# Kernel tuning notes

Hardware: AMD Instinct MI355X
Metric: run time of the kernel (lower is better)

The kernel has to match this reference:

```python
import jax, jax.numpy as jnp
import numpy as np

N_NODES = 100000
N_EDGES = 1600000
F_IN, F_HID, N_CLS = 128, 128, 16


def setup_inputs() -> dict:
    key = jax.random.key(0)
    ks = jax.random.split(key, 6)
    x = jax.random.normal(ks[0], (N_NODES, F_IN), dtype=jnp.float32)
    edge_index = jax.random.randint(ks[1], (2, N_EDGES), 0, N_NODES, dtype=jnp.int64)
    # Glorot-ish scaled weights (PyG GCNConv uses glorot init, bias zeros)
    W1 = jax.random.normal(ks[2], (F_IN, F_HID), dtype=jnp.float32) * (1.0 / np.sqrt(F_IN))
    b1 = jnp.zeros((F_HID,), dtype=jnp.float32)
    W2 = jax.random.normal(ks[3], (F_HID, N_CLS), dtype=jnp.float32) * (1.0 / np.sqrt(F_HID))
    b2 = jnp.zeros((N_CLS,), dtype=jnp.float32)
    return {"x": x, "edge_index": edge_index, "W1": W1, "b1": b1, "W2": W2, "b2": b2}


def _gcn_conv(x, src, dst, W, b, num_nodes):
    """PyG GCNConv: y = D^{-1/2} (A + I) D^{-1/2} (x W) + b.
    src/dst already include self-loops."""
    h = x @ W  # [N, F_out]
    deg = jax.ops.segment_sum(jnp.ones_like(dst, dtype=h.dtype), dst, num_segments=num_nodes)
    dis = jnp.where(deg > 0, jax.lax.rsqrt(jnp.maximum(deg, 1e-12)), 0.0)
    norm = dis[src] * dis[dst]  # [E+N]
    msg = h[src] * norm[:, None]  # gather + scale  [E+N, F_out]
    out = jax.ops.segment_sum(msg, dst, num_segments=num_nodes)  # scatter-add at targets
    return out + b


def reference(x, edge_index, W1, b1, W2, b2):
    num_nodes = x.shape[0]
    loops = jnp.arange(num_nodes, dtype=edge_index.dtype)
    src = jnp.concatenate([edge_index[0], loops])
    dst = jnp.concatenate([edge_index[1], loops])
    h = _gcn_conv(x, src, dst, W1, b1, num_nodes)
    h = jax.nn.relu(h)
    # F.dropout with training=False (eval mode) is identity
    h = _gcn_conv(h, src, dst, W2, b2, num_nodes)
    return jax.nn.log_softmax(h, axis=1)
```

## Files before the change

### kernel.cpp

```cpp
#include <hip/hip_runtime.h>
#include <math.h>

#define N_NODES 100000
#define N_EDGES 1600000
#define NBINS 391
#define NCHUNK 400
#define CHUNK 4000
#define M_H (NBINS * NCHUNK)
#define NBLK_H 611

typedef __attribute__((ext_vector_type(8))) short bf16x8;
typedef __attribute__((ext_vector_type(4))) float f32x4;
typedef __attribute__((ext_vector_type(2))) float f32x2;

__device__ __forceinline__ unsigned short f2bf(float f) {
    unsigned int u = __float_as_uint(f);
    u += 0x7FFF + ((u >> 16) & 1);
    return (unsigned short)(u >> 16);
}
__device__ __forceinline__ float bf_lo(unsigned int u) { return __uint_as_float(u << 16); }
__device__ __forceinline__ float bf_hi(unsigned int u) { return __uint_as_float(u & 0xFFFF0000u); }
__device__ __forceinline__ f32x2 bfpair(unsigned int u) {
    f32x2 r; r.x = bf_lo(u); r.y = bf_hi(u); return r;
}


__global__ __launch_bounds__(256) void passA_kernel(const int* __restrict__ dst,
                                                    int* __restrict__ H) {
    __shared__ int lh[NBINS];
    int tid = threadIdx.x, c = blockIdx.x;
    for (int i = tid; i < NBINS; i += 256) lh[i] = 0;
    __syncthreads();
    int base = c * CHUNK;
    #pragma unroll
    for (int i = 0; i < 16; ++i) {
        int o = i * 256 + tid;
        if (o < CHUNK) atomicAdd(&lh[dst[base + o] >> 8], 1);
    }
    __syncthreads();
    for (int i = tid; i < NBINS; i += 256) H[i * NCHUNK + c] = lh[i];
}

__global__ __launch_bounds__(256) void scanB1_kernel(int* __restrict__ H,
                                                     int* __restrict__ blk2) {
    __shared__ int s[256];
    int t = threadIdx.x, i = blockIdx.x * 256 + t;
    int v = (i < M_H) ? H[i] : 0;
    s[t] = v;
    __syncthreads();
    for (int off = 1; off < 256; off <<= 1) {
        int u = (t >= off) ? s[t - off] : 0;
        __syncthreads();
        s[t] += u;
        __syncthreads();
    }
    if (i < M_H) H[i] = s[t] - v;
    if (t == 255) blk2[blockIdx.x] = s[255];
}

__global__ __launch_bounds__(1024) void scanB2_kernel(int* __restrict__ blk2) {
    __shared__ int s[1024];
    int t = threadIdx.x;
    int v = (t < NBLK_H) ? blk2[t] : 0;
    s[t] = v;
    __syncthreads();
    for (int off = 1; off < 1024; off <<= 1) {
        int u = (t >= off) ? s[t - off] : 0;
        __syncthreads();
        s[t] += u;
        __syncthreads();
    }
    if (t < NBLK_H) blk2[t] = s[t] - v;
}

__global__ __launch_bounds__(256) void passC_kernel(const int* __restrict__ src,
                                                    const int* __restrict__ dst,
                                                    const int* __restrict__ H,
                                                    const int* __restrict__ blk2,
                                                    int* __restrict__ rec,
                                                    const float* __restrict__ x,
                                                    const float* __restrict__ W1,
                                                    const float* __restrict__ W2,
                                                    ushort* __restrict__ xb,
                                                    ushort* __restrict__ W1T,
                                                    ushort* __restrict__ W2T) {
    int b = blockIdx.x;
    if (b < NCHUNK) {
        __shared__ int base[NBINS];
        __shared__ int rk[NBINS];
        int tid = threadIdx.x;
        for (int i = tid; i < NBINS; i += 256) {
            int idx = i * NCHUNK + b;
            base[i] = H[idx] + blk2[idx >> 8];
            rk[i] = 0;
        }
        __syncthreads();
        int estart = b * CHUNK;
        #pragma unroll
        for (int i = 0; i < 16; ++i) {
            int o = i * 256 + tid;
            if (o < CHUNK) {
                int e = estart + o;
                int d = dst[e];
                int bin = d >> 8;
                int r = atomicAdd(&rk[bin], 1);
                rec[base[bin] + r] = src[e] | ((d & 255) << 17);
            }
        }
    } else if (b < NCHUNK + 12500) {
        int i = (b - NCHUNK) * 256 + threadIdx.x;
        float4 v = *(const float4*)&x[i * 4];
        ushort4 o;
        o.x = f2bf(v.x); o.y = f2bf(v.y); o.z = f2bf(v.z); o.w = f2bf(v.w);
        *(ushort4*)&xb[i * 4] = o;
    } else {
        int j = (b - NCHUNK - 12500) * 256 + threadIdx.x;
        if (j < 16384) {
            int k = j >> 7, n = j & 127;
            W1T[n * 128 + k] = f2bf(W1[j]);
        } else {
            int q = j - 16384;
            int k = q >> 4, n = q & 15;
            W2T[n * 128 + k] = f2bf(W2[q]);
        }
    }
}

__global__ __launch_bounds__(256) void passD_kernel(const int* __restrict__ H,
                                                    const int* __restrict__ blk2,
                                                    const int* __restrict__ rec,
                                                    int* __restrict__ col,
                                                    int* __restrict__ cnt,
                                                    float* __restrict__ dis) {
    __shared__ int fh[256];
    __shared__ int s[256];
    __shared__ int run[256];
    int b = blockIdx.x, t = threadIdx.x;
    int i0 = b * NCHUNK;
    int estart = H[i0] + blk2[i0 >> 8];
    int eend;
    if (b == NBINS - 1) eend = N_EDGES;
    else { int i1 = (b + 1) * NCHUNK; eend = H[i1] + blk2[i1 >> 8]; }
    fh[t] = 0;
    __syncthreads();
    for (int e = estart + t; e < eend; e += 256)
        atomicAdd(&fh[rec[e] >> 17], 1);
    __syncthreads();
    int v = fh[t];
    s[t] = v;
    __syncthreads();
    for (int off = 1; off < 256; off <<= 1) {
        int u = (t >= off) ? s[t - off] : 0;
        __syncthreads();
        s[t] += u;
        __syncthreads();
    }
    int node = b * 256 + t;
    int start = estart + s[t] - v;
    run[t] = start;
    if (node < N_NODES) {
        cnt[node] = start;
        dis[node] = rsqrtf((float)v + 1.0f);
    }
    __syncthreads();
    for (int e = estart + t; e < eend; e += 256) {
        int r = rec[e];
        int p = atomicAdd(&run[r >> 17], 1);
        col[p] = r & 0x1FFFF;
    }
}


__global__ __launch_bounds__(256) void gather1_kernel(const int* __restrict__ col,
                                                      const int* __restrict__ cnt,
                                                      const float* __restrict__ dis,
                                                      const unsigned int* __restrict__ xb,
                                                      unsigned int* __restrict__ xa) {
    int t = threadIdx.x;
    int node = blockIdx.x * 4 + (t >> 6);
    int lane = t & 63;
    float dn = dis[node];
    int beg = cnt[node];
    int end = (node == N_NODES - 1) ? N_EDGES : cnt[node + 1];
    unsigned int su = xb[node * 64 + lane];
    f32x2 a0 = bfpair(su) * dn;
    f32x2 a1 = {0.f, 0.f}, a2 = {0.f, 0.f}, a3 = {0.f, 0.f};
    f32x2 a4 = {0.f, 0.f}, a5 = {0.f, 0.f}, a6 = {0.f, 0.f}, a7 = {0.f, 0.f};
    int k = beg;
    for (; k + 8 <= end; k += 8) {
        int s0 = col[k], s1 = col[k + 1], s2 = col[k + 2], s3 = col[k + 3];
        int s4 = col[k + 4], s5 = col[k + 5], s6 = col[k + 6], s7 = col[k + 7];
        float w0 = dis[s0], w1 = dis[s1], w2 = dis[s2], w3 = dis[s3];
        float w4 = dis[s4], w5 = dis[s5], w6 = dis[s6], w7 = dis[s7];
        unsigned int u0 = xb[s0 * 64 + lane], u1 = xb[s1 * 64 + lane];
        unsigned int u2 = xb[s2 * 64 + lane], u3 = xb[s3 * 64 + lane];
        unsigned int u4 = xb[s4 * 64 + lane], u5 = xb[s5 * 64 + lane];
        unsigned int u6 = xb[s6 * 64 + lane], u7 = xb[s7 * 64 + lane];
        a0 += bfpair(u0) * w0;
        a1 += bfpair(u1) * w1;
        a2 += bfpair(u2) * w2;
        a3 += bfpair(u3) * w3;
        a4 += bfpair(u4) * w4;
        a5 += bfpair(u5) * w5;
        a6 += bfpair(u6) * w6;
        a7 += bfpair(u7) * w7;
    }
    for (; k + 4 <= end; k += 4) {
        int s0 = col[k], s1 = col[k + 1], s2 = col[k + 2], s3 = col[k + 3];
        float w0 = dis[s0], w1 = dis[s1], w2 = dis[s2], w3 = dis[s3];
        unsigned int u0 = xb[s0 * 64 + lane], u1 = xb[s1 * 64 + lane];
        unsigned int u2 = xb[s2 * 64 + lane], u3 = xb[s3 * 64 + lane];
        a0 += bfpair(u0) * w0;
        a1 += bfpair(u1) * w1;
        a2 += bfpair(u2) * w2;
        a3 += bfpair(u3) * w3;
    }
    for (; k < end; ++k) {
        int s = col[k];
        float w = dis[s];
        a0 += bfpair(xb[s * 64 + lane]) * w;
    }
    f32x2 r = (((a0 + a1) + (a2 + a3)) + ((a4 + a5) + (a6 + a7))) * dn;
    xa[node * 64 + lane] = (unsigned int)f2bf(r.x) | ((unsigned int)f2bf(r.y) << 16);
}


__global__ __launch_bounds__(256) void mlp_kernel(const ushort* __restrict__ xa,
                                                  const ushort* __restrict__ W1T,
                                                  const float* __restrict__ b1,
                                                  const ushort* __restrict__ W2T,
                                                  ushort* __restrict__ h2b) {
    __shared__ ushort sh[4][16][136];
    int t = threadIdx.x;
    int wave = t >> 6, lane = t & 63;
    int l = lane & 15, quad = lane >> 4;
    int m0 = blockIdx.x * 64 + wave * 16;
    bool valid = (m0 < N_NODES);
    int row = valid ? (m0 + l) : 0;

    f32x4 acc[8] = {};
    #pragma unroll
    for (int kk = 0; kk < 4; ++kk) {
        bf16x8 a = *(const bf16x8*)&xa[row * 128 + kk * 32 + quad * 8];
        #pragma unroll
        for (int nt = 0; nt < 8; ++nt) {
            bf16x8 b = *(const bf16x8*)&W1T[(nt * 16 + l) * 128 + kk * 32 + quad * 8];
            acc[nt] = __builtin_amdgcn_mfma_f32_16x16x32_bf16(a, b, acc[nt], 0, 0, 0);
        }
    }
    #pragma unroll
    for (int nt = 0; nt < 8; ++nt) {
        float bias = b1[nt * 16 + l];
        #pragma unroll
        for (int r = 0; r < 4; ++r)
            sh[wave][quad * 4 + r][nt * 16 + l] = f2bf(fmaxf(acc[nt][r] + bias, 0.0f));
    }
    __syncthreads();

    f32x4 acc2 = {};
    #pragma unroll
    for (int kk = 0; kk < 4; ++kk) {
        bf16x8 a2 = *(const bf16x8*)&sh[wave][l][kk * 32 + quad * 8];
        bf16x8 bw = *(const bf16x8*)&W2T[l * 128 + kk * 32 + quad * 8];
        acc2 = __builtin_amdgcn_mfma_f32_16x16x32_bf16(a2, bw, acc2, 0, 0, 0);
    }
    if (valid) {
        #pragma unroll
        for (int r = 0; r < 4; ++r)
            h2b[(m0 + quad * 4 + r) * 16 + l] = f2bf(acc2[r]);
    }
}


__global__ __launch_bounds__(256) void gather2_lsm_kernel(const int* __restrict__ col,
                                                          const int* __restrict__ cnt,
                                                          const float* __restrict__ dis,
                                                          const unsigned int* __restrict__ h2p,
                                                          const float* __restrict__ b2,
                                                          float* __restrict__ out) {
    int t = threadIdx.x;
    int node = blockIdx.x * 32 + (t >> 3);
    int c = t & 7;
    float dn = dis[node];
    int beg = cnt[node];
    int end = (node == N_NODES - 1) ? N_EDGES : cnt[node + 1];
    unsigned int su = h2p[node * 8 + c];
    f32x2 a0 = bfpair(su) * dn;
    f32x2 a1 = {0.f, 0.f}, a2 = {0.f, 0.f}, a3 = {0.f, 0.f};
    f32x2 a4 = {0.f, 0.f}, a5 = {0.f, 0.f}, a6 = {0.f, 0.f}, a7 = {0.f, 0.f};
    int k = beg;
    for (; k + 8 <= end; k += 8) {
        int s0 = col[k], s1 = col[k + 1], s2 = col[k + 2], s3 = col[k + 3];
        int s4 = col[k + 4], s5 = col[k + 5], s6 = col[k + 6], s7 = col[k + 7];
        float w0 = dis[s0], w1 = dis[s1], w2 = dis[s2], w3 = dis[s3];
        float w4 = dis[s4], w5 = dis[s5], w6 = dis[s6], w7 = dis[s7];
        unsigned int u0 = h2p[s0 * 8 + c], u1 = h2p[s1 * 8 + c];
        unsigned int u2 = h2p[s2 * 8 + c], u3 = h2p[s3 * 8 + c];
        unsigned int u4 = h2p[s4 * 8 + c], u5 = h2p[s5 * 8 + c];
        unsigned int u6 = h2p[s6 * 8 + c], u7 = h2p[s7 * 8 + c];
        a0 += bfpair(u0) * w0;
        a1 += bfpair(u1) * w1;
        a2 += bfpair(u2) * w2;
        a3 += bfpair(u3) * w3;
        a4 += bfpair(u4) * w4;
        a5 += bfpair(u5) * w5;
        a6 += bfpair(u6) * w6;
        a7 += bfpair(u7) * w7;
    }
    for (; k + 4 <= end; k += 4) {
        int s0 = col[k], s1 = col[k + 1], s2 = col[k + 2], s3 = col[k + 3];
        float w0 = dis[s0], w1 = dis[s1], w2 = dis[s2], w3 = dis[s3];
        unsigned int u0 = h2p[s0 * 8 + c], u1 = h2p[s1 * 8 + c];
        unsigned int u2 = h2p[s2 * 8 + c], u3 = h2p[s3 * 8 + c];
        a0 += bfpair(u0) * w0;
        a1 += bfpair(u1) * w1;
        a2 += bfpair(u2) * w2;
        a3 += bfpair(u3) * w3;
    }
    for (; k < end; ++k) {
        int s = col[k];
        float w = dis[s];
        a0 += bfpair(h2p[s * 8 + c]) * w;
    }
    f32x2 r = ((a0 + a1) + (a2 + a3)) + ((a4 + a5) + (a6 + a7));
    float2 bb = ((const float2*)b2)[c];
    float v0 = r.x * dn + bb.x;
    float v1 = r.y * dn + bb.y;
    float m = fmaxf(v0, v1);
    #pragma unroll
    for (int off = 1; off < 8; off <<= 1) m = fmaxf(m, __shfl_xor(m, off, 8));
    float ssum = expf(v0 - m) + expf(v1 - m);
    #pragma unroll
    for (int off = 1; off < 8; off <<= 1) ssum += __shfl_xor(ssum, off, 8);
    float lg = m + logf(ssum);
    ((float2*)out)[node * 8 + c] = make_float2(v0 - lg, v1 - lg);
}


extern "C" void kernel_launch(void* const* d_in, const int* in_sizes, int n_in,
                              void* d_out, int out_size, void* d_ws, size_t ws_size,
                              hipStream_t stream) {
    const float* x  = (const float*)d_in[0];
    const int*   ei = (const int*)d_in[1];
    const float* W1 = (const float*)d_in[2];
    const float* b1 = (const float*)d_in[3];
    const float* W2 = (const float*)d_in[4];
    const float* b2 = (const float*)d_in[5];
    float* out = (float*)d_out;

    const int* src = ei;
    const int* dst = ei + N_EDGES;

    char* ws = (char*)d_ws;
    ushort* xb   = (ushort*)(ws + 0);
    ushort* h2b  = (ushort*)(ws + 0);
    ushort* xa   = (ushort*)(ws + 25600000);
    int*    rec  = (int*)   (ws + 25600000);
    int*    H    = (int*)   (ws + 32000000);
    int*    col  = (int*)   (ws + 51200000);
    float*  dis  = (float*) (ws + 57600000);
    int*    cnt  = (int*)   (ws + 58000000);
    int*    blk2 = (int*)   (ws + 58400000);
    ushort* W1T  = (ushort*)(ws + 58404096);
    ushort* W2T  = (ushort*)(ws + 58436864);

    passA_kernel      <<<NCHUNK, 256, 0, stream>>>(dst, H);
    scanB1_kernel     <<<NBLK_H, 256, 0, stream>>>(H, blk2);
    scanB2_kernel     <<<1, 1024, 0, stream>>>(blk2);
    passC_kernel      <<<NCHUNK + 12500 + 72, 256, 0, stream>>>(src, dst, H, blk2, rec,
                                                                x, W1, W2, xb, W1T, W2T);
    passD_kernel      <<<NBINS, 256, 0, stream>>>(H, blk2, rec, col, cnt, dis);

    gather1_kernel    <<<N_NODES / 4, 256, 0, stream>>>(col, cnt, dis,
                                                        (const unsigned int*)xb,
                                                        (unsigned int*)xa);
    mlp_kernel        <<<1563, 256, 0, stream>>>(xa, W1T, b1, W2T, h2b);
    gather2_lsm_kernel<<<3125, 256, 0, stream>>>(col, cnt, dis,
                                                 (const unsigned int*)h2b, b2, out);
}
```

Baseline: 268.1 us.

## Prescale features by source degree norm to drop per-edge dis gathers

Computes node degrees early with global atomics in passA and derives dis in extra scanB1 blocks. The source-side normalization is then folded into the bf16 conversion of x and into the MLP output h2b, so both gather kernels accumulate unscaled rows. This removes the random per-edge dis[src] loads from both aggregation passes. In exchange it adds 1.6M global atomics on deg plus a memset, and the prescaling changes bf16 rounding slightly.

```diff
diff --git a/kernel.cpp b/kernel.cpp
--- a/kernel.cpp
+++ b/kernel.cpp
@@ -8,6 +8,7 @@
 #define CHUNK 4000
 #define M_H (NBINS * NCHUNK)
 #define NBLK_H 611
+#define NBLK_DIS 391
 
 typedef __attribute__((ext_vector_type(8))) short bf16x8;
 typedef __attribute__((ext_vector_type(4))) float f32x4;
@@ -26,7 +27,8 @@
 
 
 __global__ __launch_bounds__(256) void passA_kernel(const int* __restrict__ dst,
-                                                    int* __restrict__ H) {
+                                                    int* __restrict__ H,
+                                                    int* __restrict__ deg) {
     __shared__ int lh[NBINS];
     int tid = threadIdx.x, c = blockIdx.x;
     for (int i = tid; i < NBINS; i += 256) lh[i] = 0;
@@ -35,14 +37,25 @@
     #pragma unroll
     for (int i = 0; i < 16; ++i) {
         int o = i * 256 + tid;
-        if (o < CHUNK) atomicAdd(&lh[dst[base + o] >> 8], 1);
+        if (o < CHUNK) {
+            int d = dst[base + o];
+            atomicAdd(&lh[d >> 8], 1);
+            atomicAdd(&deg[d], 1);
+        }
     }
     __syncthreads();
     for (int i = tid; i < NBINS; i += 256) H[i * NCHUNK + c] = lh[i];
 }
 
 __global__ __launch_bounds__(256) void scanB1_kernel(int* __restrict__ H,
-                                                     int* __restrict__ blk2) {
+                                                     int* __restrict__ blk2,
+                                                     const int* __restrict__ deg,
+                                                     float* __restrict__ dis) {
+    if (blockIdx.x >= NBLK_H) {
+        int n = (blockIdx.x - NBLK_H) * 256 + threadIdx.x;
+        if (n < N_NODES) dis[n] = rsqrtf((float)deg[n] + 1.0f);
+        return;
+    }
     __shared__ int s[256];
     int t = threadIdx.x, i = blockIdx.x * 256 + t;
     int v = (i < M_H) ? H[i] : 0;
@@ -81,6 +94,7 @@
                                                     const float* __restrict__ x,
                                                     const float* __restrict__ W1,
                                                     const float* __restrict__ W2,
+                                                    const float* __restrict__ dis,
                                                     ushort* __restrict__ xb,
                                                     ushort* __restrict__ W1T,
                                                     ushort* __restrict__ W2T) {
@@ -109,9 +123,11 @@
         }
     } else if (b < NCHUNK + 12500) {
         int i = (b - NCHUNK) * 256 + threadIdx.x;
+        float dn = dis[i >> 5];
         float4 v = *(const float4*)&x[i * 4];
         ushort4 o;
-        o.x = f2bf(v.x); o.y = f2bf(v.y); o.z = f2bf(v.z); o.w = f2bf(v.w);
+        o.x = f2bf(v.x * dn); o.y = f2bf(v.y * dn);
+        o.z = f2bf(v.z * dn); o.w = f2bf(v.w * dn);
         *(ushort4*)&xb[i * 4] = o;
     } else {
         int j = (b - NCHUNK - 12500) * 256 + threadIdx.x;
@@ -130,8 +146,7 @@
                                                     const int* __restrict__ blk2,
                                                     const int* __restrict__ rec,
                                                     int* __restrict__ col,
-                                                    int* __restrict__ cnt,
-                                                    float* __restrict__ dis) {
+                                                    int* __restrict__ cnt) {
     __shared__ int fh[256];
     __shared__ int s[256];
     __shared__ int run[256];
@@ -158,10 +173,7 @@
     int node = b * 256 + t;
     int start = estart + s[t] - v;
     run[t] = start;
-    if (node < N_NODES) {
-        cnt[node] = start;
-        dis[node] = rsqrtf((float)v + 1.0f);
-    }
+    if (node < N_NODES) cnt[node] = start;
     __syncthreads();
     for (int e = estart + t; e < eend; e += 256) {
         int r = rec[e];
@@ -183,42 +195,38 @@
     int beg = cnt[node];
     int end = (node == N_NODES - 1) ? N_EDGES : cnt[node + 1];
     unsigned int su = xb[node * 64 + lane];
-    f32x2 a0 = bfpair(su) * dn;
+    f32x2 a0 = bfpair(su);
     f32x2 a1 = {0.f, 0.f}, a2 = {0.f, 0.f}, a3 = {0.f, 0.f};
     f32x2 a4 = {0.f, 0.f}, a5 = {0.f, 0.f}, a6 = {0.f, 0.f}, a7 = {0.f, 0.f};
     int k = beg;
     for (; k + 8 <= end; k += 8) {
         int s0 = col[k], s1 = col[k + 1], s2 = col[k + 2], s3 = col[k + 3];
         int s4 = col[k + 4], s5 = col[k + 5], s6 = col[k + 6], s7 = col[k + 7];
-        float w0 = dis[s0], w1 = dis[s1], w2 = dis[s2], w3 = dis[s3];
-        float w4 = dis[s4], w5 = dis[s5], w6 = dis[s6], w7 = dis[s7];
         unsigned int u0 = xb[s0 * 64 + lane], u1 = xb[s1 * 64 + lane];
         unsigned int u2 = xb[s2 * 64 + lane], u3 = xb[s3 * 64 + lane];
         unsigned int u4 = xb[s4 * 64 + lane], u5 = xb[s5 * 64 + lane];
         unsigned int u6 = xb[s6 * 64 + lane], u7 = xb[s7 * 64 + lane];
-        a0 += bfpair(u0) * w0;
-        a1 += bfpair(u1) * w1;
-        a2 += bfpair(u2) * w2;
-        a3 += bfpair(u3) * w3;
-        a4 += bfpair(u4) * w4;
-        a5 += bfpair(u5) * w5;
-        a6 += bfpair(u6) * w6;
-        a7 += bfpair(u7) * w7;
+        a0 += bfpair(u0);
+        a1 += bfpair(u1);
+        a2 += bfpair(u2);
+        a3 += bfpair(u3);
+        a4 += bfpair(u4);
+        a5 += bfpair(u5);
+        a6 += bfpair(u6);
+        a7 += bfpair(u7);
     }
     for (; k + 4 <= end; k += 4) {
         int s0 = col[k], s1 = col[k + 1], s2 = col[k + 2], s3 = col[k + 3];
-        float w0 = dis[s0], w1 = dis[s1], w2 = dis[s2], w3 = dis[s3];
         unsigned int u0 = xb[s0 * 64 + lane], u1 = xb[s1 * 64 + lane];
         unsigned int u2 = xb[s2 * 64 + lane], u3 = xb[s3 * 64 + lane];
-        a0 += bfpair(u0) * w0;
-        a1 += bfpair(u1) * w1;
-        a2 += bfpair(u2) * w2;
-        a3 += bfpair(u3) * w3;
+        a0 += bfpair(u0);
+        a1 += bfpair(u1);
+        a2 += bfpair(u2);
+        a3 += bfpair(u3);
     }
     for (; k < end; ++k) {
         int s = col[k];
-        float w = dis[s];
-        a0 += bfpair(xb[s * 64 + lane]) * w;
+        a0 += bfpair(xb[s * 64 + lane]);
     }
     f32x2 r = (((a0 + a1) + (a2 + a3)) + ((a4 + a5) + (a6 + a7))) * dn;
     xa[node * 64 + lane] = (unsigned int)f2bf(r.x) | ((unsigned int)f2bf(r.y) << 16);
@@ -229,6 +237,7 @@
                                                   const ushort* __restrict__ W1T,
                                                   const float* __restrict__ b1,
                                                   const ushort* __restrict__ W2T,
+                                                  const float* __restrict__ dis,
                                                   ushort* __restrict__ h2b) {
     __shared__ ushort sh[4][16][136];
     int t = threadIdx.x;
@@ -266,8 +275,10 @@
     }
     if (valid) {
         #pragma unroll
-        for (int r = 0; r < 4; ++r)
-            h2b[(m0 + quad * 4 + r) * 16 + l] = f2bf(acc2[r]);
+        for (int r = 0; r < 4; ++r) {
+            int m = m0 + quad * 4 + r;
+            h2b[m * 16 + l] = f2bf(acc2[r] * dis[m]);
+        }
     }
 }
 
@@ -285,42 +296,38 @@
     int beg = cnt[node];
     int end = (node == N_NODES - 1) ? N_EDGES : cnt[node + 1];
     unsigned int su = h2p[node * 8 + c];
-    f32x2 a0 = bfpair(su) * dn;
+    f32x2 a0 = bfpair(su);
     f32x2 a1 = {0.f, 0.f}, a2 = {0.f, 0.f}, a3 = {0.f, 0.f};
     f32x2 a4 = {0.f, 0.f}, a5 = {0.f, 0.f}, a6 = {0.f, 0.f}, a7 = {0.f, 0.f};
     int k = beg;
     for (; k + 8 <= end; k += 8) {
         int s0 = col[k], s1 = col[k + 1], s2 = col[k + 2], s3 = col[k + 3];
         int s4 = col[k + 4], s5 = col[k + 5], s6 = col[k + 6], s7 = col[k + 7];
-        float w0 = dis[s0], w1 = dis[s1], w2 = dis[s2], w3 = dis[s3];
-        float w4 = dis[s4], w5 = dis[s5], w6 = dis[s6], w7 = dis[s7];
         unsigned int u0 = h2p[s0 * 8 + c], u1 = h2p[s1 * 8 + c];
         unsigned int u2 = h2p[s2 * 8 + c], u3 = h2p[s3 * 8 + c];
         unsigned int u4 = h2p[s4 * 8 + c], u5 = h2p[s5 * 8 + c];
         unsigned int u6 = h2p[s6 * 8 + c], u7 = h2p[s7 * 8 + c];
-        a0 += bfpair(u0) * w0;
-        a1 += bfpair(u1) * w1;
-        a2 += bfpair(u2) * w2;
-        a3 += bfpair(u3) * w3;
-        a4 += bfpair(u4) * w4;
-        a5 += bfpair(u5) * w5;
-        a6 += bfpair(u6) * w6;
-        a7 += bfpair(u7) * w7;
+        a0 += bfpair(u0);
+        a1 += bfpair(u1);
+        a2 += bfpair(u2);
+        a3 += bfpair(u3);
+        a4 += bfpair(u4);
+        a5 += bfpair(u5);
+        a6 += bfpair(u6);
+        a7 += bfpair(u7);
     }
     for (; k + 4 <= end; k += 4) {
         int s0 = col[k], s1 = col[k + 1], s2 = col[k + 2], s3 = col[k + 3];
-        float w0 = dis[s0], w1 = dis[s1], w2 = dis[s2], w3 = dis[s3];
         unsigned int u0 = h2p[s0 * 8 + c], u1 = h2p[s1 * 8 + c];
         unsigned int u2 = h2p[s2 * 8 + c], u3 = h2p[s3 * 8 + c];
-        a0 += bfpair(u0) * w0;
-        a1 += bfpair(u1) * w1;
-        a2 += bfpair(u2) * w2;
-        a3 += bfpair(u3) * w3;
+        a0 += bfpair(u0);
+        a1 += bfpair(u1);
+        a2 += bfpair(u2);
+        a3 += bfpair(u3);
     }
     for (; k < end; ++k) {
         int s = col[k];
-        float w = dis[s];
-        a0 += bfpair(h2p[s * 8 + c]) * w;
+        a0 += bfpair(h2p[s * 8 + c]);
     }
     f32x2 r = ((a0 + a1) + (a2 + a3)) + ((a4 + a5) + (a6 + a7));
     float2 bb = ((const float2*)b2)[c];
@@ -358,23 +365,26 @@
     int*    rec  = (int*)   (ws + 25600000);
     int*    H    = (int*)   (ws + 32000000);
     int*    col  = (int*)   (ws + 51200000);
+    int*    deg  = (int*)   (ws + 51200000);
     float*  dis  = (float*) (ws + 57600000);
     int*    cnt  = (int*)   (ws + 58000000);
     int*    blk2 = (int*)   (ws + 58400000);
     ushort* W1T  = (ushort*)(ws + 58404096);
     ushort* W2T  = (ushort*)(ws + 58436864);
 
-    passA_kernel      <<<NCHUNK, 256, 0, stream>>>(dst, H);
-    scanB1_kernel     <<<NBLK_H, 256, 0, stream>>>(H, blk2);
+    hipMemsetAsync(deg, 0, N_NODES * sizeof(int), stream);
+    passA_kernel      <<<NCHUNK, 256, 0, stream>>>(dst, H, deg);
+    scanB1_kernel     <<<NBLK_H + NBLK_DIS, 256, 0, stream>>>(H, blk2, deg, dis);
     scanB2_kernel     <<<1, 1024, 0, stream>>>(blk2);
     passC_kernel      <<<NCHUNK + 12500 + 72, 256, 0, stream>>>(src, dst, H, blk2, rec,
-                                                                x, W1, W2, xb, W1T, W2T);
-    passD_kernel      <<<NBINS, 256, 0, stream>>>(H, blk2, rec, col, cnt, dis);
+                                                                x, W1, W2, dis,
+                                                                xb, W1T, W2T);
+    passD_kernel      <<<NBINS, 256, 0, stream>>>(H, blk2, rec, col, cnt);
 
     gather1_kernel    <<<N_NODES / 4, 256, 0, stream>>>(col, cnt, dis,
                                                         (const unsigned int*)xb,
                                                         (unsigned int*)xa);
-    mlp_kernel        <<<1563, 256, 0, stream>>>(xa, W1T, b1, W2T, h2b);
+    mlp_kernel        <<<1563, 256, 0, stream>>>(xa, W1T, b1, W2T, dis, h2b);
     gather2_lsm_kernel<<<3125, 256, 0, stream>>>(col, cnt, dis,
                                                  (const unsigned int*)h2b, b2, out);
 }
```

Result: slower. 325.4 us (+21.4%).
